# Kernel tuning notes

Hardware: AMD Instinct MI355X
Metric: run time of the kernel (lower is better)

Reference implementation:

```python
import jax, jax.numpy as jnp
import numpy as np

N = 100000      # nodes
E = 1600000     # edges (before self-loops)
IN = 128        # in_channels
H = 4           # heads
C = 32          # hidden_channels (per head)
HC = H * C      # 128, LayerNorm dim
NEG_SLOPE = 0.2
LN_EPS = 1e-5


def setup_inputs() -> dict:
    key = jax.random.key(0)
    ks = jax.random.split(key, 8)
    x = jax.random.normal(ks[0], (N, IN), dtype=jnp.float32)
    edge_index = jax.random.randint(ks[1], (2, E), 0, N, dtype=jnp.int64)
    edge_weight = jax.random.uniform(ks[2], (E,), dtype=jnp.float32)
    # GATConv parameters
    W = jax.random.normal(ks[3], (IN, HC), dtype=jnp.float32) * (1.0 / np.sqrt(IN))
    att_src = jax.random.normal(ks[4], (H, C), dtype=jnp.float32) * (1.0 / np.sqrt(C))
    att_dst = jax.random.normal(ks[5], (H, C), dtype=jnp.float32) * (1.0 / np.sqrt(C))
    bias = jnp.zeros((HC,), dtype=jnp.float32)
    # LayerNorm parameters
    gamma = jnp.ones((HC,), dtype=jnp.float32)
    beta = jnp.zeros((HC,), dtype=jnp.float32)
    return {"x": x, "edge_index": edge_index, "edge_weight": edge_weight,
            "W": W, "att_src": att_src, "att_dst": att_dst, "bias": bias,
            "gamma": gamma, "beta": beta}


def reference(x, edge_index, edge_weight, W, att_src, att_dst, bias, gamma, beta):
    # --- GATConv (heads=4, concat, add_self_loops=True) ---
    loops = jnp.arange(N, dtype=edge_index.dtype)
    ei = jnp.concatenate([edge_index, jnp.stack([loops, loops])], axis=1)  # [2, E+N]
    src, dst = ei[0], ei[1]

    xw = (x @ W).reshape(N, H, C)                       # [N, H, C]
    a_src = jnp.sum(xw * att_src, axis=-1)              # [N, H]
    a_dst = jnp.sum(xw * att_dst, axis=-1)              # [N, H]

    # per-edge attention logits, softmax grouped by destination node
    e = jax.nn.leaky_relu(a_src[src] + a_dst[dst], NEG_SLOPE)   # [E+N, H]
    m = jax.ops.segment_max(e, dst, num_segments=N)             # [N, H]
    ex = jnp.exp(e - m[dst])
    denom = jax.ops.segment_sum(ex, dst, num_segments=N)        # [N, H]
    alpha = ex / (denom[dst] + 1e-16)                           # [E+N, H]

    # weighted scatter-add of source features to destinations
    msg = alpha[:, :, None] * xw[src]                           # [E+N, H, C]
    out = jax.ops.segment_sum(msg, dst, num_segments=N)         # [N, H, C]
    out = out.reshape(N, HC) + bias                             # concat heads + bias

    # --- LayerNorm ---
    mu = jnp.mean(out, axis=-1, keepdims=True)
    var = jnp.var(out, axis=-1, keepdims=True)
    return gamma * (out - mu) / jnp.sqrt(var + LN_EPS) + beta
```

## Files before the change

### kernel.cpp

```cpp
#include <hip/hip_runtime.h>
#include <math.h>

#define NN 100000
#define EE 1600000
#define ETOT (EE + NN)
#define NBUK 512
#define NPB 196
#define CHUNK 3125
#define CAP 6144

typedef __attribute__((ext_vector_type(8))) short bf16x8;
typedef __attribute__((ext_vector_type(4))) float f32x4;

__device__ __forceinline__ unsigned short f2bf(float f) {
  unsigned int u = __float_as_uint(f);
  u = u + 0x7fffu + ((u >> 16) & 1u);
  return (unsigned short)(u >> 16);
}

__device__ __forceinline__ float lrelu_exp(float e) {
  e = (e > 0.f) ? e : 0.2f * e;
  return __expf(e);
}

__global__ __launch_bounds__(256) void k_gemm(const float* __restrict__ x,
                                              const float* __restrict__ W,
                                              unsigned short* __restrict__ xwb) {
  __shared__ __align__(16) unsigned short lds[17408];
  int tid = threadIdx.x;
  for (int i = tid; i < 16384; i += 256) {
    int k = i >> 7, n = i & 127;
    lds[n * 136 + k] = f2bf(W[i]);
  }
  __syncthreads();

  int wv = tid >> 6, lane = tid & 63;
  int m = lane & 15, q = lane >> 4;
  int r = blockIdx.x * 64 + wv * 16 + m;
  bool rok = (r < NN);

  bf16x8 af[4];
#pragma unroll
  for (int kt = 0; kt < 4; kt++) {
    float4 v0 = make_float4(0.f, 0.f, 0.f, 0.f), v1 = v0;
    if (rok) {
      v0 = ((const float4*)x)[(size_t)r * 32 + kt * 8 + q * 2];
      v1 = ((const float4*)x)[(size_t)r * 32 + kt * 8 + q * 2 + 1];
    }
    af[kt][0] = (short)f2bf(v0.x); af[kt][1] = (short)f2bf(v0.y);
    af[kt][2] = (short)f2bf(v0.z); af[kt][3] = (short)f2bf(v0.w);
    af[kt][4] = (short)f2bf(v1.x); af[kt][5] = (short)f2bf(v1.y);
    af[kt][6] = (short)f2bf(v1.z); af[kt][7] = (short)f2bf(v1.w);
  }

  f32x4 acc[8];
#pragma unroll
  for (int nt = 0; nt < 8; nt++) acc[nt] = (f32x4){0.f, 0.f, 0.f, 0.f};

#pragma unroll
  for (int nt = 0; nt < 8; nt++) {
#pragma unroll
    for (int kt = 0; kt < 4; kt++) {
      bf16x8 bf = *((const bf16x8*)&lds[(nt * 16 + m) * 136 + kt * 32 + q * 8]);
      acc[nt] = __builtin_amdgcn_mfma_f32_16x16x32_bf16(af[kt], bf, acc[nt], 0, 0, 0);
    }
  }

  __syncthreads();
#pragma unroll
  for (int nt = 0; nt < 8; nt++)
#pragma unroll
    for (int rg = 0; rg < 4; rg++)
      lds[(wv * 16 + q * 4 + rg) * 128 + nt * 16 + m] = f2bf(acc[nt][rg]);
  __syncthreads();

  size_t base = (size_t)blockIdx.x * 16384;
  const size_t lim = (size_t)NN * 256;
  for (int i = tid; i < 1024; i += 256) {
    size_t off = base + (size_t)i * 16;
    if (off < lim) *((uint4*)((char*)xwb + off)) = ((const uint4*)lds)[i];
  }
}

__global__ __launch_bounds__(256) void k_logit(const unsigned short* __restrict__ xwb,
                                               const float* __restrict__ att_src,
                                               const float* __restrict__ att_dst,
                                               float* __restrict__ a) {
  __shared__ float att[256];
  int tid = threadIdx.x;
  if (tid < 128) att[tid] = att_src[tid];
  else if (tid < 256) att[tid] = att_dst[tid - 128];
  __syncthreads();
  int g = blockIdx.x * 256 + tid;
  int node = g >> 2, h = g & 3;
  if (node >= NN) return;
  const uint4* row = (const uint4*)(xwb + (size_t)node * 128) + h * 4;
  float ss = 0.f, sd = 0.f;
#pragma unroll
  for (int cq = 0; cq < 4; cq++) {
    uint4 u = row[cq];
    int cb = h * 32 + cq * 8;
    float f0 = __uint_as_float(u.x << 16), f1 = __uint_as_float(u.x & 0xffff0000u);
    float f2 = __uint_as_float(u.y << 16), f3 = __uint_as_float(u.y & 0xffff0000u);
    float f4 = __uint_as_float(u.z << 16), f5 = __uint_as_float(u.z & 0xffff0000u);
    float f6 = __uint_as_float(u.w << 16), f7 = __uint_as_float(u.w & 0xffff0000u);
    ss += f0 * att[cb] + f1 * att[cb + 1] + f2 * att[cb + 2] + f3 * att[cb + 3] +
          f4 * att[cb + 4] + f5 * att[cb + 5] + f6 * att[cb + 6] + f7 * att[cb + 7];
    sd += f0 * att[128 + cb] + f1 * att[128 + cb + 1] + f2 * att[128 + cb + 2] +
          f3 * att[128 + cb + 3] + f4 * att[128 + cb + 4] + f5 * att[128 + cb + 5] +
          f6 * att[128 + cb + 6] + f7 * att[128 + cb + 7];
  }
  a[(size_t)node * 8 + h] = ss;
  a[(size_t)node * 8 + 4 + h] = sd;
}

__global__ __launch_bounds__(256) void k_p1(const int* __restrict__ ei,
                                            int* __restrict__ H) {
  __shared__ int h[NBUK];
  int j = blockIdx.x, t = threadIdx.x;
  for (int i = t; i < NBUK; i += 256) h[i] = 0;
  __syncthreads();
  int e0 = j * CHUNK;
  for (int e = e0 + t; e < e0 + CHUNK; e += 256) {
    int d = ei[(size_t)EE + e];
    atomicAdd(&h[d / NPB], 1);
  }
  __syncthreads();
  for (int i = t; i < NBUK; i += 256) H[j * NBUK + i] = h[i];
}

__global__ __launch_bounds__(512) void k_s1(const int* __restrict__ H,
                                            int* __restrict__ R, int* __restrict__ T) {
  __shared__ int s[512];
  int b = blockIdx.x, t = threadIdx.x;
  int v = H[t * NBUK + b];
  s[t] = v;
  __syncthreads();
  for (int off = 1; off < 512; off <<= 1) {
    int tmp = (t >= off) ? s[t - off] : 0;
    __syncthreads();
    s[t] += tmp;
    __syncthreads();
  }
  R[b * 512 + t] = s[t] - v;
  if (t == 511) T[b] = s[511];
}

__global__ __launch_bounds__(512) void k_s2(const int* __restrict__ T,
                                            int* __restrict__ BaseTmp,
                                            int* __restrict__ Base) {
  __shared__ int s[512];
  __shared__ int s2[512];
  int t = threadIdx.x;
  int v = T[t];
  int ncnt = NN - t * NPB;
  ncnt = (ncnt < 0) ? 0 : ((ncnt > NPB) ? NPB : ncnt);
  int w = v + ncnt;
  s[t] = v; s2[t] = w;
  __syncthreads();
  for (int off = 1; off < 512; off <<= 1) {
    int ta = (t >= off) ? s[t - off] : 0;
    int tb = (t >= off) ? s2[t - off] : 0;
    __syncthreads();
    s[t] += ta; s2[t] += tb;
    __syncthreads();
  }
  BaseTmp[t] = s[t] - v;
  Base[t] = s2[t] - w;
}

__global__ __launch_bounds__(256) void k_p3(const int* __restrict__ ei,
                                            const int* __restrict__ R,
                                            const int* __restrict__ BaseTmp,
                                            int* __restrict__ tmpb) {
  __shared__ int cur[NBUK];
  int j = blockIdx.x, t = threadIdx.x;
  for (int b = t; b < NBUK; b += 256) cur[b] = BaseTmp[b] + R[b * 512 + j];
  __syncthreads();
  int e0 = j * CHUNK;
  for (int e = e0 + t; e < e0 + CHUNK; e += 256) {
    int s = ei[e];
    int d = ei[(size_t)EE + e];
    int b = d / NPB;
    int li = d - b * NPB;
    int pos = atomicAdd(&cur[b], 1);
    tmpb[pos] = (li << 17) | s;
  }
}

__global__ __launch_bounds__(256) void k_p4(const int* __restrict__ tmpb,
                                            const int* __restrict__ T,
                                            const int* __restrict__ BaseTmp,
                                            const int* __restrict__ Base,
                                            const float* __restrict__ a,
                                            int* __restrict__ es, int* __restrict__ offs,
                                            float* __restrict__ ew,
                                            float* __restrict__ na) {
  __shared__ int cnt[256];
  __shared__ int cur[NPB];
  __shared__ int stage[CAP];
  __shared__ float ssum[NPB * 4];
  int b = blockIdx.x, t = threadIdx.x;
  if (b == 0 && t == 0) offs[NN] = ETOT;
  int n0 = b * NPB;
  int nloc = NN - n0;
  if (nloc <= 0) return;
  if (nloc > NPB) nloc = NPB;
  int total = T[b];
  int bt = BaseTmp[b], bs = Base[b];
  cnt[t] = (t < nloc) ? 1 : 0;
  for (int i = t; i < NPB * 4; i += 256) ssum[i] = 0.f;
  __syncthreads();
  for (int e = t; e < total; e += 256) {
    int u = tmpb[bt + e];
    atomicAdd(&cnt[u >> 17], 1);
  }
  __syncthreads();
  int v = cnt[t];
  __syncthreads();
  for (int off = 1; off < 256; off <<= 1) {
    int tmp = (t >= off) ? cnt[t - off] : 0;
    __syncthreads();
    cnt[t] += tmp;
    __syncthreads();
  }
  int excl = cnt[t] - v;
  if (t < nloc) {
    int node = n0 + t;
    offs[node] = bs + excl;
    cur[t] = excl + 1;
    if (excl < CAP) {
      stage[excl] = node;
      float4 asv = *((const float4*)(a + (size_t)node * 8));
      float4 adv = *((const float4*)(a + (size_t)node * 8 + 4));
      float4 w4;
      w4.x = lrelu_exp(asv.x + adv.x); w4.y = lrelu_exp(asv.y + adv.y);
      w4.z = lrelu_exp(asv.z + adv.z); w4.w = lrelu_exp(asv.w + adv.w);
      *((float4*)(ew + (size_t)(bs + excl) * 4)) = w4;
      atomicAdd(&ssum[t * 4 + 0], w4.x); atomicAdd(&ssum[t * 4 + 1], w4.y);
      atomicAdd(&ssum[t * 4 + 2], w4.z); atomicAdd(&ssum[t * 4 + 3], w4.w);
    }
  }
  __syncthreads();
  for (int e = t; e < total; e += 256) {
    int u = tmpb[bt + e];
    int li = u >> 17;
    int src = u & 0x1FFFF;
    int pos = atomicAdd(&cur[li], 1);
    if (pos < CAP) {
      stage[pos] = src;
      float4 asv = *((const float4*)(a + (size_t)src * 8));
      float4 adv = *((const float4*)(a + (size_t)(n0 + li) * 8 + 4));
      float4 w4;
      w4.x = lrelu_exp(asv.x + adv.x); w4.y = lrelu_exp(asv.y + adv.y);
      w4.z = lrelu_exp(asv.z + adv.z); w4.w = lrelu_exp(asv.w + adv.w);
      *((float4*)(ew + (size_t)(bs + pos) * 4)) = w4;
      atomicAdd(&ssum[li * 4 + 0], w4.x); atomicAdd(&ssum[li * 4 + 1], w4.y);
      atomicAdd(&ssum[li * 4 + 2], w4.z); atomicAdd(&ssum[li * 4 + 3], w4.w);
    }
  }
  __syncthreads();
  int btot = total + nloc;
  if (btot > CAP) btot = CAP;
  for (int i = t; i < btot; i += 256) es[bs + i] = stage[i];
  for (int i = t; i < nloc * 4; i += 256)
    na[(size_t)n0 * 4 + i] = 1.f / (ssum[i] + 1e-16f);
}

__global__ __launch_bounds__(256) void k_agg(const unsigned short* __restrict__ xwb,
                                             const float* __restrict__ ew,
                                             const float* __restrict__ na,
                                             const int* __restrict__ offs,
                                             const int* __restrict__ es,
                                             const float* __restrict__ bias,
                                             const float* __restrict__ gamma,
                                             const float* __restrict__ beta,
                                             float* __restrict__ out) {
  int lane = threadIdx.x & 63;
  int node = blockIdx.x * 4 + (threadIdx.x >> 6);
  int off0 = offs[node];
  int d = offs[node + 1] - off0;
  int h = lane >> 4;
  int c = lane * 2;
  float rn = na[(size_t)node * 4 + h];

  const unsigned* xp = (const unsigned*)xwb + lane;
  const int* ep = es + off0;
  const float* wp = ew + (size_t)off0 * 4 + h;
  float ax0 = 0.f, ay0 = 0.f, ax1 = 0.f, ay1 = 0.f;

  int j = 0;
  for (; j + 4 <= d; j += 4) {
    int4 sp = *((const int4*)(ep + j));
    float w0 = wp[4 * j];
    float w1 = wp[4 * j + 4];
    float w2 = wp[4 * j + 8];
    float w3 = wp[4 * j + 12];
    unsigned u0 = xp[(unsigned)sp.x * 64u];
    unsigned u1 = xp[(unsigned)sp.y * 64u];
    unsigned u2 = xp[(unsigned)sp.z * 64u];
    unsigned u3 = xp[(unsigned)sp.w * 64u];
    ax0 = fmaf(w0, __uint_as_float(u0 << 16), ax0);
    ay0 = fmaf(w0, __uint_as_float(u0 & 0xffff0000u), ay0);
    ax1 = fmaf(w1, __uint_as_float(u1 << 16), ax1);
    ay1 = fmaf(w1, __uint_as_float(u1 & 0xffff0000u), ay1);
    ax0 = fmaf(w2, __uint_as_float(u2 << 16), ax0);
    ay0 = fmaf(w2, __uint_as_float(u2 & 0xffff0000u), ay0);
    ax1 = fmaf(w3, __uint_as_float(u3 << 16), ax1);
    ay1 = fmaf(w3, __uint_as_float(u3 & 0xffff0000u), ay1);
  }
  for (; j < d; ++j) {
    int s0 = ep[j];
    float w0 = wp[4 * j];
    unsigned u0 = xp[(unsigned)s0 * 64u];
    ax0 = fmaf(w0, __uint_as_float(u0 << 16), ax0);
    ay0 = fmaf(w0, __uint_as_float(u0 & 0xffff0000u), ay0);
  }
  float accx = ax0 + ax1, accy = ay0 + ay1;

  float vx = accx * rn + bias[c];
  float vy = accy * rn + bias[c + 1];
  float sum = vx + vy, sq = vx * vx + vy * vy;
#pragma unroll
  for (int o = 32; o; o >>= 1) {
    sum += __shfl_xor(sum, o);
    sq += __shfl_xor(sq, o);
  }
  float mean = sum * (1.f / 128.f);
  float var = sq * (1.f / 128.f) - mean * mean;
  float rs = rsqrtf(var + 1e-5f);
  float o0 = gamma[c] * (vx - mean) * rs + beta[c];
  float o1 = gamma[c + 1] * (vy - mean) * rs + beta[c + 1];
  float2 ov; ov.x = o0; ov.y = o1;
  *((float2*)(out + (size_t)node * 128 + c)) = ov;
}

extern "C" void kernel_launch(void* const* d_in, const int* in_sizes, int n_in,
                              void* d_out, int out_size, void* d_ws, size_t ws_size,
                              hipStream_t stream) {
  const float* x = (const float*)d_in[0];
  const int* ei = (const int*)d_in[1];
  const float* W = (const float*)d_in[3];
  const float* att_src = (const float*)d_in[4];
  const float* att_dst = (const float*)d_in[5];
  const float* bias = (const float*)d_in[6];
  const float* gamma = (const float*)d_in[7];
  const float* beta = (const float*)d_in[8];
  float* out = (float*)d_out;

  char* p = (char*)d_ws;
  auto alloc = [&](size_t bytes) -> char* {
    char* r = p;
    p += (bytes + 255) & ~(size_t)255;
    return r;
  };
  unsigned short* xwb = (unsigned short*)alloc((size_t)NN * 128 * 2);
  float* a = (float*)alloc((size_t)NN * 8 * 4);
  int* es = (int*)alloc((size_t)ETOT * 4);
  int* offs = (int*)alloc((size_t)(NN + 1) * 4);
  float* ew = (float*)alloc((size_t)ETOT * 4 * 4);
  float* na = (float*)alloc((size_t)NN * 4 * 4);
  int* tmpb = (int*)alloc((size_t)EE * 4);
  int* H = (int*)alloc((size_t)512 * NBUK * 4);
  int* R = (int*)alloc((size_t)NBUK * 512 * 4);
  int* T = (int*)alloc((size_t)NBUK * 4);
  int* BaseTmp = (int*)alloc((size_t)(NBUK + 1) * 4);
  int* Base = (int*)alloc((size_t)(NBUK + 1) * 4);

  k_gemm<<<(NN + 63) / 64, 256, 0, stream>>>(x, W, xwb);
  k_logit<<<(NN * 4 + 255) / 256, 256, 0, stream>>>(xwb, att_src, att_dst, a);
  k_p1<<<512, 256, 0, stream>>>(ei, H);
  k_s1<<<NBUK, 512, 0, stream>>>(H, R, T);
  k_s2<<<1, 512, 0, stream>>>(T, BaseTmp, Base);
  k_p3<<<512, 256, 0, stream>>>(ei, R, BaseTmp, tmpb);
  k_p4<<<NBUK, 256, 0, stream>>>(tmpb, T, BaseTmp, Base, a, es, offs, ew, na);
  k_agg<<<NN / 4, 256, 0, stream>>>(xwb, ew, na, offs, es, bias, gamma, beta, out);
}
```

Measured before the change: 302.3 us.

## Fuse attention logits into GEMM and recompute edge weights in aggregation

The attention-logit computation moves into the GEMM epilogue, reading bf16 xw from LDS, so the separate logit kernel and its reload of xw are gone. Source and destination logits are now stored as separate arrays. The per-edge exp weight array (about 27 MB written by p4 and read by agg) is dropped. k_agg recomputes each weight with a gathered asrc load plus exp, and its loop is unrolled by 8 to keep more gathers in flight. The trade is extra exp work and random 4-byte gathers in the aggregation in exchange for less memory traffic and one fewer launch.

```diff
diff --git a/kernel.cpp b/kernel.cpp
--- a/kernel.cpp
+++ b/kernel.cpp
@@ -25,13 +25,20 @@
 
 __global__ __launch_bounds__(256) void k_gemm(const float* __restrict__ x,
                                               const float* __restrict__ W,
-                                              unsigned short* __restrict__ xwb) {
+                                              const float* __restrict__ att_src,
+                                              const float* __restrict__ att_dst,
+                                              unsigned short* __restrict__ xwb,
+                                              float* __restrict__ asrc,
+                                              float* __restrict__ adst) {
   __shared__ __align__(16) unsigned short lds[17408];
+  __shared__ float satt[256];
   int tid = threadIdx.x;
   for (int i = tid; i < 16384; i += 256) {
     int k = i >> 7, n = i & 127;
     lds[n * 136 + k] = f2bf(W[i]);
   }
+  if (tid < 128) satt[tid] = att_src[tid];
+  else satt[tid] = att_dst[tid - 128];
   __syncthreads();
 
   int wv = tid >> 6, lane = tid & 63;
@@ -80,38 +87,28 @@
     size_t off = base + (size_t)i * 16;
     if (off < lim) *((uint4*)((char*)xwb + off)) = ((const uint4*)lds)[i];
   }
-}
-
-__global__ __launch_bounds__(256) void k_logit(const unsigned short* __restrict__ xwb,
-                                               const float* __restrict__ att_src,
-                                               const float* __restrict__ att_dst,
-                                               float* __restrict__ a) {
-  __shared__ float att[256];
-  int tid = threadIdx.x;
-  if (tid < 128) att[tid] = att_src[tid];
-  else if (tid < 256) att[tid] = att_dst[tid - 128];
-  __syncthreads();
-  int g = blockIdx.x * 256 + tid;
-  int node = g >> 2, h = g & 3;
-  if (node >= NN) return;
-  const uint4* row = (const uint4*)(xwb + (size_t)node * 128) + h * 4;
-  float ss = 0.f, sd = 0.f;
-#pragma unroll
-  for (int cq = 0; cq < 4; cq++) {
-    uint4 u = row[cq];
-    int cb = h * 32 + cq * 8;
-    float f0 = __uint_as_float(u.x << 16), f1 = __uint_as_float(u.x & 0xffff0000u);
-    float f2 = __uint_as_float(u.y << 16), f3 = __uint_as_float(u.y & 0xffff0000u);
-    float f4 = __uint_as_float(u.z << 16), f5 = __uint_as_float(u.z & 0xffff0000u);
-    float f6 = __uint_as_float(u.w << 16), f7 = __uint_as_float(u.w & 0xffff0000u);
-    ss += f0 * att[cb] + f1 * att[cb + 1] + f2 * att[cb + 2] + f3 * att[cb + 3] +
-          f4 * att[cb + 4] + f5 * att[cb + 5] + f6 * att[cb + 6] + f7 * att[cb + 7];
-    sd += f0 * att[128 + cb] + f1 * att[128 + cb + 1] + f2 * att[128 + cb + 2] +
-          f3 * att[128 + cb + 3] + f4 * att[128 + cb + 4] + f5 * att[128 + cb + 5] +
-          f6 * att[128 + cb + 6] + f7 * att[128 + cb + 7];
-  }
-  a[(size_t)node * 8 + h] = ss;
-  a[(size_t)node * 8 + 4 + h] = sd;
+
+  int row = tid >> 2, h = tid & 3;
+  int node = blockIdx.x * 64 + row;
+  if (node < NN) {
+    float ss = 0.f, sd = 0.f;
+#pragma unroll
+    for (int cq = 0; cq < 4; cq++) {
+      uint4 u = *((const uint4*)&lds[row * 128 + h * 32 + cq * 8]);
+      int cb = h * 32 + cq * 8;
+      float f0 = __uint_as_float(u.x << 16), f1 = __uint_as_float(u.x & 0xffff0000u);
+      float f2 = __uint_as_float(u.y << 16), f3 = __uint_as_float(u.y & 0xffff0000u);
+      float f4 = __uint_as_float(u.z << 16), f5 = __uint_as_float(u.z & 0xffff0000u);
+      float f6 = __uint_as_float(u.w << 16), f7 = __uint_as_float(u.w & 0xffff0000u);
+      ss += f0 * satt[cb] + f1 * satt[cb + 1] + f2 * satt[cb + 2] + f3 * satt[cb + 3] +
+            f4 * satt[cb + 4] + f5 * satt[cb + 5] + f6 * satt[cb + 6] + f7 * satt[cb + 7];
+      sd += f0 * satt[128 + cb] + f1 * satt[128 + cb + 1] + f2 * satt[128 + cb + 2] +
+            f3 * satt[128 + cb + 3] + f4 * satt[128 + cb + 4] + f5 * satt[128 + cb + 5] +
+            f6 * satt[128 + cb + 6] + f7 * satt[128 + cb + 7];
+    }
+    asrc[(size_t)node * 4 + h] = ss;
+    adst[(size_t)node * 4 + h] = sd;
+  }
 }
 
 __global__ __launch_bounds__(256) void k_p1(const int* __restrict__ ei,
@@ -192,14 +189,15 @@
                                             const int* __restrict__ T,
                                             const int* __restrict__ BaseTmp,
                                             const int* __restrict__ Base,
-                                            const float* __restrict__ a,
+                                            const float* __restrict__ asrc,
+                                            const float* __restrict__ adst,
                                             int* __restrict__ es, int* __restrict__ offs,
-                                            float* __restrict__ ew,
                                             float* __restrict__ na) {
   __shared__ int cnt[256];
   __shared__ int cur[NPB];
   __shared__ int stage[CAP];
-  __shared__ float ssum[NPB * 4];
+  __shared__ __align__(16) float ssum[NPB * 4];
+  __shared__ __align__(16) float adl[NPB * 4];
   int b = blockIdx.x, t = threadIdx.x;
   if (b == 0 && t == 0) offs[NN] = ETOT;
   int n0 = b * NPB;
@@ -210,6 +208,7 @@
   int bt = BaseTmp[b], bs = Base[b];
   cnt[t] = (t < nloc) ? 1 : 0;
   for (int i = t; i < NPB * 4; i += 256) ssum[i] = 0.f;
+  for (int i = t; i < nloc * 4; i += 256) adl[i] = adst[(size_t)n0 * 4 + i];
   __syncthreads();
   for (int e = t; e < total; e += 256) {
     int u = tmpb[bt + e];
@@ -231,12 +230,11 @@
     cur[t] = excl + 1;
     if (excl < CAP) {
       stage[excl] = node;
-      float4 asv = *((const float4*)(a + (size_t)node * 8));
-      float4 adv = *((const float4*)(a + (size_t)node * 8 + 4));
+      float4 asv = *((const float4*)(asrc + (size_t)node * 4));
+      float4 adv = *((const float4*)&adl[t * 4]);
       float4 w4;
       w4.x = lrelu_exp(asv.x + adv.x); w4.y = lrelu_exp(asv.y + adv.y);
       w4.z = lrelu_exp(asv.z + adv.z); w4.w = lrelu_exp(asv.w + adv.w);
-      *((float4*)(ew + (size_t)(bs + excl) * 4)) = w4;
       atomicAdd(&ssum[t * 4 + 0], w4.x); atomicAdd(&ssum[t * 4 + 1], w4.y);
       atomicAdd(&ssum[t * 4 + 2], w4.z); atomicAdd(&ssum[t * 4 + 3], w4.w);
     }
@@ -249,12 +247,11 @@
     int pos = atomicAdd(&cur[li], 1);
     if (pos < CAP) {
       stage[pos] = src;
-      float4 asv = *((const float4*)(a + (size_t)src * 8));
-      float4 adv = *((const float4*)(a + (size_t)(n0 + li) * 8 + 4));
+      float4 asv = *((const float4*)(asrc + (size_t)src * 4));
+      float4 adv = *((const float4*)&adl[li * 4]);
       float4 w4;
       w4.x = lrelu_exp(asv.x + adv.x); w4.y = lrelu_exp(asv.y + adv.y);
       w4.z = lrelu_exp(asv.z + adv.z); w4.w = lrelu_exp(asv.w + adv.w);
-      *((float4*)(ew + (size_t)(bs + pos) * 4)) = w4;
       atomicAdd(&ssum[li * 4 + 0], w4.x); atomicAdd(&ssum[li * 4 + 1], w4.y);
       atomicAdd(&ssum[li * 4 + 2], w4.z); atomicAdd(&ssum[li * 4 + 3], w4.w);
     }
@@ -268,7 +265,8 @@
 }
 
 __global__ __launch_bounds__(256) void k_agg(const unsigned short* __restrict__ xwb,
-                                             const float* __restrict__ ew,
+                                             const float* __restrict__ asrc,
+                                             const float* __restrict__ adst,
                                              const float* __restrict__ na,
                                              const int* __restrict__ offs,
                                              const int* __restrict__ es,
@@ -283,38 +281,39 @@
   int h = lane >> 4;
   int c = lane * 2;
   float rn = na[(size_t)node * 4 + h];
+  float ad = adst[(size_t)node * 4 + h];
 
   const unsigned* xp = (const unsigned*)xwb + lane;
   const int* ep = es + off0;
-  const float* wp = ew + (size_t)off0 * 4 + h;
   float ax0 = 0.f, ay0 = 0.f, ax1 = 0.f, ay1 = 0.f;
 
   int j = 0;
-  for (; j + 4 <= d; j += 4) {
-    int4 sp = *((const int4*)(ep + j));
-    float w0 = wp[4 * j];
-    float w1 = wp[4 * j + 4];
-    float w2 = wp[4 * j + 8];
-    float w3 = wp[4 * j + 12];
-    unsigned u0 = xp[(unsigned)sp.x * 64u];
-    unsigned u1 = xp[(unsigned)sp.y * 64u];
-    unsigned u2 = xp[(unsigned)sp.z * 64u];
-    unsigned u3 = xp[(unsigned)sp.w * 64u];
-    ax0 = fmaf(w0, __uint_as_float(u0 << 16), ax0);
-    ay0 = fmaf(w0, __uint_as_float(u0 & 0xffff0000u), ay0);
-    ax1 = fmaf(w1, __uint_as_float(u1 << 16), ax1);
-    ay1 = fmaf(w1, __uint_as_float(u1 & 0xffff0000u), ay1);
-    ax0 = fmaf(w2, __uint_as_float(u2 << 16), ax0);
-    ay0 = fmaf(w2, __uint_as_float(u2 & 0xffff0000u), ay0);
-    ax1 = fmaf(w3, __uint_as_float(u3 << 16), ax1);
-    ay1 = fmaf(w3, __uint_as_float(u3 & 0xffff0000u), ay1);
+  for (; j + 8 <= d; j += 8) {
+    int4 sa = *((const int4*)(ep + j));
+    int4 sb = *((const int4*)(ep + j + 4));
+    int sv[8] = {sa.x, sa.y, sa.z, sa.w, sb.x, sb.y, sb.z, sb.w};
+    float av[8];
+    unsigned uu[8];
+#pragma unroll
+    for (int q = 0; q < 8; q++) {
+      av[q] = asrc[(size_t)(unsigned)sv[q] * 4 + h];
+      uu[q] = xp[(unsigned)sv[q] * 64u];
+    }
+#pragma unroll
+    for (int q = 0; q < 8; q++) {
+      float w = lrelu_exp(av[q] + ad);
+      float lo = __uint_as_float(uu[q] << 16);
+      float hi = __uint_as_float(uu[q] & 0xffff0000u);
+      if (q & 1) { ax1 = fmaf(w, lo, ax1); ay1 = fmaf(w, hi, ay1); }
+      else       { ax0 = fmaf(w, lo, ax0); ay0 = fmaf(w, hi, ay0); }
+    }
   }
   for (; j < d; ++j) {
     int s0 = ep[j];
-    float w0 = wp[4 * j];
+    float w = lrelu_exp(asrc[(size_t)(unsigned)s0 * 4 + h] + ad);
     unsigned u0 = xp[(unsigned)s0 * 64u];
-    ax0 = fmaf(w0, __uint_as_float(u0 << 16), ax0);
-    ay0 = fmaf(w0, __uint_as_float(u0 & 0xffff0000u), ay0);
+    ax0 = fmaf(w, __uint_as_float(u0 << 16), ax0);
+    ay0 = fmaf(w, __uint_as_float(u0 & 0xffff0000u), ay0);
   }
   float accx = ax0 + ax1, accy = ay0 + ay1;
 
@@ -355,10 +354,10 @@
     return r;
   };
   unsigned short* xwb = (unsigned short*)alloc((size_t)NN * 128 * 2);
-  float* a = (float*)alloc((size_t)NN * 8 * 4);
+  float* asrc = (float*)alloc((size_t)NN * 4 * 4);
+  float* adst = (float*)alloc((size_t)NN * 4 * 4);
   int* es = (int*)alloc((size_t)ETOT * 4);
   int* offs = (int*)alloc((size_t)(NN + 1) * 4);
-  float* ew = (float*)alloc((size_t)ETOT * 4 * 4);
   float* na = (float*)alloc((size_t)NN * 4 * 4);
   int* tmpb = (int*)alloc((size_t)EE * 4);
   int* H = (int*)alloc((size_t)512 * NBUK * 4);
@@ -367,12 +366,11 @@
   int* BaseTmp = (int*)alloc((size_t)(NBUK + 1) * 4);
   int* Base = (int*)alloc((size_t)(NBUK + 1) * 4);
 
-  k_gemm<<<(NN + 63) / 64, 256, 0, stream>>>(x, W, xwb);
-  k_logit<<<(NN * 4 + 255) / 256, 256, 0, stream>>>(xwb, att_src, att_dst, a);
+  k_gemm<<<(NN + 63) / 64, 256, 0, stream>>>(x, W, att_src, att_dst, xwb, asrc, adst);
   k_p1<<<512, 256, 0, stream>>>(ei, H);
   k_s1<<<NBUK, 512, 0, stream>>>(H, R, T);
   k_s2<<<1, 512, 0, stream>>>(T, BaseTmp, Base);
   k_p3<<<512, 256, 0, stream>>>(ei, R, BaseTmp, tmpb);
-  k_p4<<<NBUK, 256, 0, stream>>>(tmpb, T, BaseTmp, Base, a, es, offs, ew, na);
-  k_agg<<<NN / 4, 256, 0, stream>>>(xwb, ew, na, offs, es, bias, gamma, beta, out);
-}
+  k_p4<<<NBUK, 256, 0, stream>>>(tmpb, T, BaseTmp, Base, asrc, adst, es, offs, na);
+  k_agg<<<NN / 4, 256, 0, stream>>>(xwb, asrc, adst, na, offs, es, bias, gamma, beta, out);
+}
```

Result: no change. 302.6 us (+0.1%).
